# Kernel tuning notes

Hardware: AMD Instinct MI355X
Metric: run time of the kernel (lower is better)

## Reference

```python
import jax, jax.numpy as jnp
import numpy as np

NUM_MODULES = 4
EXPERTS_PER_MODULE = 4
TOTAL_EXPERTS = NUM_MODULES * EXPERTS_PER_MODULE
TOP_K = 4
NORM_TOPK_PROB = True
T = 32768
D = 1536


def setup_inputs() -> dict:
    key = jax.random.key(0)
    k1, k2, k3 = jax.random.split(key, 3)
    hidden_states = jax.random.normal(k1, (T, D), dtype=jnp.float32)
    # nn.Linear weights: (out_features, in_features)
    Wm = jax.random.normal(k2, (NUM_MODULES, D), dtype=jnp.float32) * 0.02
    We = jax.random.normal(k3, (TOTAL_EXPERTS, D), dtype=jnp.float32) * 0.02
    return {"hidden_states": hidden_states, "Wm": Wm, "We": We}


def reference(hidden_states, Wm, We):
    Tn = hidden_states.shape[0]
    # Stage 1: module routing
    module_logits = jnp.einsum('td,md->tm', hidden_states, Wm)  # (T, num_modules)
    module_probs = jax.nn.softmax(module_logits.astype(jnp.float32), axis=-1)
    # Stage 2: expert routing, grouped per module (intra-module softmax)
    expert_logits = jnp.einsum('td,ed->te', hidden_states, We)  # (T, total_experts)
    expert_logits = expert_logits.reshape(Tn, NUM_MODULES, EXPERTS_PER_MODULE)
    expert_probs = jax.nn.softmax(expert_logits.astype(jnp.float32), axis=-1)
    # Combined hierarchical distribution
    combined_probs = (module_probs[:, :, None] * expert_probs).reshape(Tn, TOTAL_EXPERTS)
    # Top-k over flat combined distribution
    top_k_weights, top_k_indices = jax.lax.top_k(combined_probs, TOP_K)
    if NORM_TOPK_PROB:
        top_k_weights = top_k_weights / (jnp.sum(top_k_weights, axis=-1, keepdims=True) + 1e-8)
    top_k_weights = top_k_weights.astype(hidden_states.dtype)
    return combined_probs, top_k_weights, top_k_indices
```

## Files before the change

### kernel.cpp

```cpp
#include <hip/hip_runtime.h>
#include <math.h>


#define DD 1536
#define NM 4
#define NE 16
#define NW 20
#define RPB 64
#define NWAVE 8
#define NTHR (NWAVE * 64)
#define CPW 192
#define CHUNK 16
#define NCHUNK (CPW / CHUNK)
#define LSTRIDE 20
#define HS_FLOATS (RPB * LSTRIDE)
#define W_FLOATS  (NW * LSTRIDE)
#define WAVE_REG  (HS_FLOATS + W_FLOATS)

typedef float v4f __attribute__((ext_vector_type(4)));

union SharedMem {
    float stage[NWAVE * WAVE_REG];
    float xch[NW * NTHR];
};

__global__ __launch_bounds__(NTHR)
void router_kernel(const float* __restrict__ hs,
                   const float* __restrict__ Wm,
                   const float* __restrict__ We,
                   float* __restrict__ out,
                   int T)
{
    __shared__ SharedMem sm;
    const int tid  = threadIdx.x;
    const int wv   = tid >> 6;
    const int lane = tid & 63;
    const int rowBlock = blockIdx.x * RPB;
    const int colStart = wv * CPW;

    float acc[NW];
#pragma unroll
    for (int e = 0; e < NW; e++) acc[e] = 0.f;

    const int srow = lane >> 2;
    const int scol = (lane & 3) << 2;
    const float* hsBase = hs + (size_t)(rowBlock + srow) * DD + colStart + scol;
    float* myHs = &sm.stage[wv * WAVE_REG];
    float* myW  = myHs + HS_FLOATS;

    const int wrow0 = lane >> 2;
    const int wgrp0 = (lane & 3) << 2;
    const float* weBase = We + (size_t)wrow0 * DD + colStart + wgrp0;
    const float* wmBase = Wm + (size_t)(lane >> 2) * DD + colStart + wgrp0;

    v4f hbuf[4], wbuf0, wbuf1;
#pragma unroll
    for (int i = 0; i < 4; i++)
        hbuf[i] = *(const v4f*)(hsBase + (size_t)(i * 16) * DD);
    wbuf0 = *(const v4f*)(weBase);
    if (lane < 16) wbuf1 = *(const v4f*)(wmBase);

    for (int c = 0; c < CPW; c += CHUNK) {
#pragma unroll
        for (int i = 0; i < 4; i++)
            *(v4f*)&myHs[(srow + i * 16) * LSTRIDE + scol] = hbuf[i];
        *(v4f*)&myW[wrow0 * LSTRIDE + wgrp0] = wbuf0;
        if (lane < 16)
            *(v4f*)&myW[(16 + (lane >> 2)) * LSTRIDE + wgrp0] = wbuf1;

        if (c + CHUNK < CPW) {
            const int cn = c + CHUNK;
#pragma unroll
            for (int i = 0; i < 4; i++)
                hbuf[i] = *(const v4f*)(hsBase + (size_t)(i * 16) * DD + cn);
            wbuf0 = *(const v4f*)(weBase + cn);
            if (lane < 16) wbuf1 = *(const v4f*)(wmBase + cn);
        }

#pragma unroll
        for (int g = 0; g < 4; g++) {
            v4f h = *(const v4f*)&myHs[lane * LSTRIDE + (g << 2)];
#pragma unroll
            for (int e = 0; e < NW; e++) {
                v4f w = *(const v4f*)&myW[e * LSTRIDE + (g << 2)];
                acc[e] += h.x * w.x + h.y * w.y + h.z * w.z + h.w * w.w;
            }
        }
    }

    __syncthreads();
#pragma unroll
    for (int e = 0; e < NW; e++) sm.xch[e * NTHR + tid] = acc[e];
    __syncthreads();

    if (wv == 0) {
        float logit[NW];
#pragma unroll
        for (int e = 0; e < NW; e++) {
            float s = 0.f;
#pragma unroll
            for (int w = 0; w < NWAVE; w++)
                s += sm.xch[e * NTHR + w * 64 + lane];
            logit[e] = s;
        }

        float mmax = logit[16];
#pragma unroll
        for (int m = 1; m < NM; m++) mmax = fmaxf(mmax, logit[16 + m]);
        float mexp[NM], msum = 0.f;
#pragma unroll
        for (int m = 0; m < NM; m++) { mexp[m] = expf(logit[16 + m] - mmax); msum += mexp[m]; }

        float comb[NE];
#pragma unroll
        for (int m = 0; m < NM; m++) {
            float mprob = mexp[m] / msum;
            float emax = logit[m * 4];
#pragma unroll
            for (int j = 1; j < 4; j++) emax = fmaxf(emax, logit[m * 4 + j]);
            float ee[4], esum = 0.f;
#pragma unroll
            for (int j = 0; j < 4; j++) { ee[j] = expf(logit[m * 4 + j] - emax); esum += ee[j]; }
            float scale = mprob / esum;
#pragma unroll
            for (int j = 0; j < 4; j++) comb[m * 4 + j] = ee[j] * scale;
        }

        const int row = rowBlock + lane;
        float4* cw = (float4*)(out + (size_t)row * 16);
        cw[0] = make_float4(comb[0],  comb[1],  comb[2],  comb[3]);
        cw[1] = make_float4(comb[4],  comb[5],  comb[6],  comb[7]);
        cw[2] = make_float4(comb[8],  comb[9],  comb[10], comb[11]);
        cw[3] = make_float4(comb[12], comb[13], comb[14], comb[15]);

        float tv[4]; int ti[4];
        unsigned mask = 0;
#pragma unroll
        for (int k = 0; k < 4; k++) {
            float best = -1.f; int bi = 0;
#pragma unroll
            for (int i = 0; i < NE; i++) {
                bool avail = !((mask >> i) & 1u);
                if (avail && comb[i] > best) { best = comb[i]; bi = i; }
            }
            tv[k] = best; ti[k] = bi; mask |= 1u << bi;
        }
        float s = tv[0] + tv[1] + tv[2] + tv[3] + 1e-8f;

        const size_t wOff = (size_t)T * 16;
        const size_t iOff = (size_t)T * 20;
        float4* ww = (float4*)(out + wOff + (size_t)row * 4);
        *ww = make_float4(tv[0] / s, tv[1] / s, tv[2] / s, tv[3] / s);
        float4* iw = (float4*)(out + iOff + (size_t)row * 4);
        *iw = make_float4((float)ti[0], (float)ti[1], (float)ti[2], (float)ti[3]);
    }
}

extern "C" void kernel_launch(void* const* d_in, const int* in_sizes, int n_in,
                              void* d_out, int out_size, void* d_ws, size_t ws_size,
                              hipStream_t stream)
{
    const float* hs = (const float*)d_in[0];
    const float* Wm = (const float*)d_in[1];
    const float* We = (const float*)d_in[2];
    float* out = (float*)d_out;
    const int T = in_sizes[0] / DD;
    router_kernel<<<T / RPB, NTHR, 0, stream>>>(hs, Wm, We, out, T);
}
```

Measured before the change: 295.4 us.

## Process 128 rows per block with two accumulator sets per lane

Doubles the rows handled per block from 64 to 128. Each lane now keeps two sets of 20 accumulators, so every weight vector read from LDS serves two hidden rows, and the cross-wave reduction plus softmax/top-k epilogue is split across two waves. This cuts LDS weight reads per FLOP and halves the block count. In exchange it raises register use, which may lower occupancy, and it doubles the LDS exchange buffer to 80KB.

```diff
diff --git a/kernel.cpp b/kernel.cpp
--- a/kernel.cpp
+++ b/kernel.cpp
@@ -6,12 +6,11 @@
 #define NM 4
 #define NE 16
 #define NW 20
-#define RPB 64
+#define RPB 128
 #define NWAVE 8
 #define NTHR (NWAVE * 64)
 #define CPW 192
 #define CHUNK 16
-#define NCHUNK (CPW / CHUNK)
 #define LSTRIDE 20
 #define HS_FLOATS (RPB * LSTRIDE)
 #define W_FLOATS  (NW * LSTRIDE)
@@ -21,7 +20,7 @@
 
 union SharedMem {
     float stage[NWAVE * WAVE_REG];
-    float xch[NW * NTHR];
+    float xch[NW * NTHR * 2];
 };
 
 __global__ __launch_bounds__(NTHR)
@@ -38,9 +37,9 @@
     const int rowBlock = blockIdx.x * RPB;
     const int colStart = wv * CPW;
 
-    float acc[NW];
+    float acc0[NW], acc1[NW];
 #pragma unroll
-    for (int e = 0; e < NW; e++) acc[e] = 0.f;
+    for (int e = 0; e < NW; e++) { acc0[e] = 0.f; acc1[e] = 0.f; }
 
     const int srow = lane >> 2;
     const int scol = (lane & 3) << 2;
@@ -48,30 +47,28 @@
     float* myHs = &sm.stage[wv * WAVE_REG];
     float* myW  = myHs + HS_FLOATS;
 
-    const int wrow0 = lane >> 2;
-    const int wgrp0 = (lane & 3) << 2;
-    const float* weBase = We + (size_t)wrow0 * DD + colStart + wgrp0;
-    const float* wmBase = Wm + (size_t)(lane >> 2) * DD + colStart + wgrp0;
+    const float* weBase = We + (size_t)srow * DD + colStart + scol;
+    const float* wmBase = Wm + (size_t)srow * DD + colStart + scol;
 
-    v4f hbuf[4], wbuf0, wbuf1;
+    v4f hbuf[8], wbuf0, wbuf1;
 #pragma unroll
-    for (int i = 0; i < 4; i++)
+    for (int i = 0; i < 8; i++)
         hbuf[i] = *(const v4f*)(hsBase + (size_t)(i * 16) * DD);
     wbuf0 = *(const v4f*)(weBase);
     if (lane < 16) wbuf1 = *(const v4f*)(wmBase);
 
     for (int c = 0; c < CPW; c += CHUNK) {
 #pragma unroll
-        for (int i = 0; i < 4; i++)
+        for (int i = 0; i < 8; i++)
             *(v4f*)&myHs[(srow + i * 16) * LSTRIDE + scol] = hbuf[i];
-        *(v4f*)&myW[wrow0 * LSTRIDE + wgrp0] = wbuf0;
+        *(v4f*)&myW[srow * LSTRIDE + scol] = wbuf0;
         if (lane < 16)
-            *(v4f*)&myW[(16 + (lane >> 2)) * LSTRIDE + wgrp0] = wbuf1;
+            *(v4f*)&myW[(16 + srow) * LSTRIDE + scol] = wbuf1;
 
         if (c + CHUNK < CPW) {
             const int cn = c + CHUNK;
 #pragma unroll
-            for (int i = 0; i < 4; i++)
+            for (int i = 0; i < 8; i++)
                 hbuf[i] = *(const v4f*)(hsBase + (size_t)(i * 16) * DD + cn);
             wbuf0 = *(const v4f*)(weBase + cn);
             if (lane < 16) wbuf1 = *(const v4f*)(wmBase + cn);
@@ -79,28 +76,34 @@
 
 #pragma unroll
         for (int g = 0; g < 4; g++) {
-            v4f h = *(const v4f*)&myHs[lane * LSTRIDE + (g << 2)];
+            v4f h0 = *(const v4f*)&myHs[lane * LSTRIDE + (g << 2)];
+            v4f h1 = *(const v4f*)&myHs[(64 + lane) * LSTRIDE + (g << 2)];
 #pragma unroll
             for (int e = 0; e < NW; e++) {
                 v4f w = *(const v4f*)&myW[e * LSTRIDE + (g << 2)];
-                acc[e] += h.x * w.x + h.y * w.y + h.z * w.z + h.w * w.w;
+                acc0[e] += h0.x * w.x + h0.y * w.y + h0.z * w.z + h0.w * w.w;
+                acc1[e] += h1.x * w.x + h1.y * w.y + h1.z * w.z + h1.w * w.w;
             }
         }
     }
 
     __syncthreads();
 #pragma unroll
-    for (int e = 0; e < NW; e++) sm.xch[e * NTHR + tid] = acc[e];
+    for (int e = 0; e < NW; e++) {
+        sm.xch[e * (NTHR * 2) + tid]        = acc0[e];
+        sm.xch[e * (NTHR * 2) + NTHR + tid] = acc1[e];
+    }
     __syncthreads();
 
-    if (wv == 0) {
+    if (wv < 2) {
+        const int half = wv * NTHR;
         float logit[NW];
 #pragma unroll
         for (int e = 0; e < NW; e++) {
             float s = 0.f;
 #pragma unroll
             for (int w = 0; w < NWAVE; w++)
-                s += sm.xch[e * NTHR + w * 64 + lane];
+                s += sm.xch[e * (NTHR * 2) + half + w * 64 + lane];
             logit[e] = s;
         }
 
@@ -126,7 +129,7 @@
             for (int j = 0; j < 4; j++) comb[m * 4 + j] = ee[j] * scale;
         }
 
-        const int row = rowBlock + lane;
+        const int row = rowBlock + wv * 64 + lane;
         float4* cw = (float4*)(out + (size_t)row * 16);
         cw[0] = make_float4(comb[0],  comb[1],  comb[2],  comb[3]);
         cw[1] = make_float4(comb[4],  comb[5],  comb[6],  comb[7]);
```

Result: slower. 377.7 us (+27.9%).
